# Performance work log

Hardware: AMD Instinct MI355X
Metric: run time of the kernel (lower is better)

## Reference

```python
import jax, jax.numpy as jnp
import numpy as np

B, S, D, H = 4, 2048, 1024, 16
HD = D // H  # head_dim = 64


def setup_inputs() -> dict:
    key = jax.random.key(0)
    ks = jax.random.split(key, 5)
    scale = 1.0 / np.sqrt(D)
    return {
        "x": jax.random.normal(ks[0], (B, S, D), dtype=jnp.float32),
        "Wq": jax.random.normal(ks[1], (D, D), dtype=jnp.float32) * scale,
        "bq": jnp.zeros((D,), dtype=jnp.float32),
        "Wk": jax.random.normal(ks[2], (D, D), dtype=jnp.float32) * scale,
        "bk": jnp.zeros((D,), dtype=jnp.float32),
        "Wv": jax.random.normal(ks[3], (D, D), dtype=jnp.float32) * scale,
        "bv": jnp.zeros((D,), dtype=jnp.float32),
        "Wp": jax.random.normal(ks[4], (D, D), dtype=jnp.float32) * scale,
        "bp": jnp.zeros((D,), dtype=jnp.float32),
    }


def reference(x, Wq, bq, Wk, bk, Wv, bv, Wp, bp):
    b, s, d = x.shape
    # qkv projections (torch Linear: x @ W.T + b; here W stored as (in,out))
    q = (x @ Wq + bq).reshape(b, s, H, HD).transpose(0, 2, 1, 3)  # (b,h,s,hd)
    k = (x @ Wk + bk).reshape(b, s, H, HD).transpose(0, 2, 1, 3)
    v = (x @ Wv + bv).reshape(b, s, H, HD).transpose(0, 2, 1, 3)
    scores = jnp.einsum("bhqd,bhkd->bhqk", q, k) / np.sqrt(HD)
    causal = jnp.tril(jnp.ones((s, s), dtype=bool))
    scores = jnp.where(causal, scores, -jnp.inf)
    attn = jax.nn.softmax(scores, axis=-1)  # dropout is identity (p=0 / eval)
    out = jnp.einsum("bhqk,bhkd->bhqd", attn, v)
    out = out.transpose(0, 2, 1, 3).reshape(b, s, d)
    return out @ Wp + bp
```

## Files before the change

### kernel.cpp

```cpp
#include <hip/hip_runtime.h>

typedef __bf16 bf16;
typedef __attribute__((ext_vector_type(4))) __bf16 bf16x4;
typedef __attribute__((ext_vector_type(8))) __bf16 bf16x8;
typedef __attribute__((ext_vector_type(4))) float f32x4;
typedef __attribute__((ext_vector_type(4))) unsigned int u32x4;

#define B_ 4
#define S_ 2048
#define D_ 1024
#define H_ 16
#define HD_ 64

#define GLB(p) ((const __attribute__((address_space(1))) void*)(p))
#define LDS(p) ((__attribute__((address_space(3))) void*)(p))

__global__ __launch_bounds__(256) void transpose_cvt(
    const float* __restrict__ W0, const float* __restrict__ W1,
    const float* __restrict__ W2, const float* __restrict__ W3,
    bf16* __restrict__ T0, bf16* __restrict__ T1,
    bf16* __restrict__ T2, bf16* __restrict__ T3)
{
    __shared__ float tile[32][33];
    int z = blockIdx.z;
    const float* W = (z == 0) ? W0 : (z == 1) ? W1 : (z == 2) ? W2 : W3;
    bf16*        T = (z == 0) ? T0 : (z == 1) ? T1 : (z == 2) ? T2 : T3;
    int bx = blockIdx.x * 32, by = blockIdx.y * 32;
    int tx = threadIdx.x & 31, ty = threadIdx.x >> 5;
    #pragma unroll
    for (int j = 0; j < 32; j += 8)
        tile[ty + j][tx] = W[(size_t)(by + ty + j) * D_ + bx + tx];
    __syncthreads();
    #pragma unroll
    for (int j = 0; j < 32; j += 8)
        T[(size_t)(bx + ty + j) * D_ + by + tx] = (bf16)tile[tx][ty + j];
}

__global__ __launch_bounds__(256) void cvt_x(
    const float* __restrict__ X, bf16* __restrict__ Xb)
{
    size_t i = ((size_t)blockIdx.x * 256 + threadIdx.x) * 8;
    f32x4 a = *(const f32x4*)(X + i);
    f32x4 b = *(const f32x4*)(X + i + 4);
    bf16x8 v;
    #pragma unroll
    for (int j = 0; j < 4; ++j) { v[j] = (bf16)a[j]; v[4 + j] = (bf16)b[j]; }
    *(bf16x8*)(Xb + i) = v;
}

__global__ __launch_bounds__(256) void qkv_gemm(
    const bf16* __restrict__ Xb,
    const bf16* __restrict__ WqT, const bf16* __restrict__ WkT, const bf16* __restrict__ WvT,
    const float* __restrict__ bq, const float* __restrict__ bk, const float* __restrict__ bv,
    bf16* __restrict__ Qo, bf16* __restrict__ Ko, bf16* __restrict__ Vo)
{
    const int lin = blockIdx.x + (blockIdx.y << 3) + (blockIdx.z << 9);
    const int xcd = lin & 7, rest = lin >> 3;
    const int byb = xcd * 8 + (rest & 7);
    const int bxb = (rest >> 3) & 7;
    const int z   = rest >> 6;

    const bf16*  WT   = (z == 0) ? WqT : (z == 1) ? WkT : WvT;
    const float* bias = (z == 0) ? bq  : (z == 1) ? bk  : bv;
    bf16*        out  = (z == 0) ? Qo  : (z == 1) ? Ko  : Vo;
    const float scale = (z == 0) ? 0.18033688011112042f : 1.0f;

    __shared__ bf16 As[128 * 64];
    __shared__ bf16 Bs[128 * 64];

    const int t = threadIdx.x;
    const int lid = t & 63, w = t >> 6;
    const int wm = w & 1, wn = w >> 1;
    const int lrow = lid & 15, quad = lid >> 4;
    const int m0 = byb * 128, n0 = bxb * 128;

    const bf16* Ag = Xb + (size_t)m0 * D_;
    const bf16* Bg = WT + (size_t)n0 * D_;

    const int srow = t >> 3;
    const int ssel = ((t & 7) ^ (srow & 7)) << 3;

    const int rsw = lrow & 7;

    f32x4 acc[4][4] = {};

    for (int k0 = 0; k0 < D_; k0 += 64) {
        __syncthreads();
        #pragma unroll
        for (int j = 0; j < 4; ++j) {
            __builtin_amdgcn_global_load_lds(
                GLB(Ag + (size_t)(srow + j * 32) * D_ + k0 + ssel),
                LDS((char*)As + j * 4096 + t * 16), 16, 0, 0);
            __builtin_amdgcn_global_load_lds(
                GLB(Bg + (size_t)(srow + j * 32) * D_ + k0 + ssel),
                LDS((char*)Bs + j * 4096 + t * 16), 16, 0, 0);
        }
        __syncthreads();
        #pragma unroll
        for (int kk = 0; kk < 2; ++kk) {
            const int ro = ((kk * 4 + quad) ^ rsw) << 4;
            bf16x8 a[4], b[4];
            #pragma unroll
            for (int mb = 0; mb < 4; ++mb)
                a[mb] = *(const bf16x8*)((const char*)As + (wm * 64 + mb * 16 + lrow) * 128 + ro);
            #pragma unroll
            for (int nb = 0; nb < 4; ++nb)
                b[nb] = *(const bf16x8*)((const char*)Bs + (wn * 64 + nb * 16 + lrow) * 128 + ro);
            #pragma unroll
            for (int mb = 0; mb < 4; ++mb)
                #pragma unroll
                for (int nb = 0; nb < 4; ++nb)
                    acc[mb][nb] = __builtin_amdgcn_mfma_f32_16x16x32_bf16(a[mb], b[nb], acc[mb][nb], 0, 0, 0);
        }
    }

    #pragma unroll
    for (int mb = 0; mb < 4; ++mb) {
        #pragma unroll
        for (int nb = 0; nb < 4; ++nb) {
            int gn = n0 + wn * 64 + nb * 16 + lrow;
            float bsv = bias[gn];
            int h = gn >> 6, hd = gn & 63;
            int gm0 = m0 + wm * 64 + mb * 16 + quad * 4;
            int bb = gm0 >> 11, s0 = gm0 & 2047;
            if (z == 2) {
                bf16x4 pk;
                #pragma unroll
                for (int r = 0; r < 4; ++r)
                    pk[r] = (bf16)(acc[mb][nb][r] + bsv);
                *(bf16x4*)(out + (((size_t)(bb * H_ + h)) * HD_ + hd) * S_ + s0) = pk;
            } else {
                #pragma unroll
                for (int r = 0; r < 4; ++r) {
                    float v = (acc[mb][nb][r] + bsv) * scale;
                    out[(((size_t)(bb * H_ + h)) * S_ + (s0 + r)) * HD_ + hd] = (bf16)v;
                }
            }
        }
    }
}

__global__ __launch_bounds__(256) void attn_fwd(
    const bf16* __restrict__ Q, const bf16* __restrict__ K,
    const bf16* __restrict__ Vt, bf16* __restrict__ O)
{
    __shared__ bf16 Ks[64 * 64];
    __shared__ bf16 Vs[64 * 64];
    __shared__ bf16 Ps[4][16 * 64];

    const int lin = blockIdx.x + (blockIdx.y << 4);
    const int xcd = lin & 7;
    const int sl  = lin >> 3;
    const int bh  = xcd * 8 + (sl >> 4);
    const int bxp = sl & 15;

    const int t = threadIdx.x, lid = t & 63, w = t >> 6;
    const int lrow = lid & 15, quad = lid >> 4;
    const int b = bh >> 4, h = bh & 15;

    const int swz = (lrow & 7) << 4;

    const int srow0 = t >> 3, srow1 = srow0 + 32;
    const int k8 = (t & 7) << 3;
    const int sswz = ((t & 7) << 4) ^ ((srow0 & 7) << 4);
    char* kdst0 = (char*)Ks + srow0 * 128 + sswz;
    char* kdst1 = (char*)Ks + srow1 * 128 + sswz;
    char* vdst0 = (char*)Vs + srow0 * 128 + sswz;
    char* vdst1 = (char*)Vs + srow1 * 128 + sswz;

    bf16x8 onesv;
    #pragma unroll
    for (int j = 0; j < 8; ++j) onesv[j] = (bf16)1.0f;

    #pragma unroll 1
    for (int half = 0; half < 2; ++half) {
        const int qtile = half ? bxp : (31 - bxp);
        const int qbase = qtile * 64;

        const bf16* Qp = Q + ((size_t)bh * S_ + qbase + w * 16) * HD_;
        bf16x8 qf[2];
        #pragma unroll
        for (int ks = 0; ks < 2; ++ks)
            qf[ks] = *(const bf16x8*)(Qp + lrow * HD_ + ks * 32 + quad * 8);

        f32x4 o_acc[4] = {};
        f32x4 l_acc = {0.0f, 0.0f, 0.0f, 0.0f};
        float m_i = -3.0e4f;

        for (int kt = 0; kt <= qtile; ++kt) {
            const bf16* Kp = K  + ((size_t)bh * S_ + kt * 64) * HD_;
            const bf16* Vp = Vt + ((size_t)bh * HD_) * S_ + kt * 64;
            __syncthreads();
            u32x4 kv0 = *(const u32x4*)(Kp + (size_t)srow0 * HD_ + k8);
            u32x4 kv1 = *(const u32x4*)(Kp + (size_t)srow1 * HD_ + k8);
            u32x4 vv0 = *(const u32x4*)(Vp + (size_t)srow0 * S_ + k8);
            u32x4 vv1 = *(const u32x4*)(Vp + (size_t)srow1 * S_ + k8);
            *(u32x4*)kdst0 = kv0;
            *(u32x4*)kdst1 = kv1;
            *(u32x4*)vdst0 = vv0;
            *(u32x4*)vdst1 = vv1;
            __syncthreads();

            f32x4 sa[4] = {};
            #pragma unroll
            for (int ks = 0; ks < 2; ++ks) {
                const int ro = ((ks << 6) + (quad << 4)) ^ swz;
                #pragma unroll
                for (int nb = 0; nb < 4; ++nb) {
                    bf16x8 kf = *(const bf16x8*)((const char*)Ks + (nb * 16 + lrow) * 128 + ro);
                    sa[nb] = __builtin_amdgcn_mfma_f32_16x16x32_bf16(kf, qf[ks], sa[nb], 0, 0, 0);
                }
            }

            if (kt == qtile) {
                int q = qbase + w * 16 + lrow;
                #pragma unroll
                for (int nb = 0; nb < 4; ++nb) {
                    int key = kt * 64 + nb * 16 + quad * 4;
                    #pragma unroll
                    for (int r = 0; r < 4; ++r)
                        if (key + r > q) sa[nb][r] = -3.0e4f;
                }
            }

            float p[4][4];
            {
                #pragma unroll
                for (int nb = 0; nb < 4; ++nb)
                    #pragma unroll
                    for (int r = 0; r < 4; ++r)
                        p[nb][r] = __builtin_amdgcn_exp2f(sa[nb][r] - m_i);

                float r0 = fmaxf(fmaxf(sa[0][0], sa[0][1]), sa[0][2]);
                float r1 = fmaxf(fmaxf(sa[0][3], sa[1][0]), sa[1][1]);
                float r2 = fmaxf(fmaxf(sa[1][2], sa[1][3]), sa[2][0]);
                float r3 = fmaxf(fmaxf(sa[2][1], sa[2][2]), sa[2][3]);
                float r4 = fmaxf(fmaxf(sa[3][0], sa[3][1]), sa[3][2]);
                float rm = fmaxf(fmaxf(fmaxf(r0, r1), r2),
                                 fmaxf(fmaxf(r3, r4), sa[3][3]));

                if (!__all(rm <= m_i + 8.0f)) {
                    rm = fmaxf(rm, __shfl_xor(rm, 16));
                    rm = fmaxf(rm, __shfl_xor(rm, 32));
                    float mnew = fmaxf(m_i, rm);
                    float al = __builtin_amdgcn_exp2f(m_i - mnew);
                    m_i = mnew;
                    #pragma unroll
                    for (int nb = 0; nb < 4; ++nb)
                        #pragma unroll
                        for (int r = 0; r < 4; ++r) {
                            o_acc[nb][r] *= al;
                            p[nb][r] = __builtin_amdgcn_exp2f(sa[nb][r] - m_i);
                        }
                    #pragma unroll
                    for (int r = 0; r < 4; ++r)
                        l_acc[r] *= al;
                }
            }

            char* pw = (char*)Ps[w] + lrow * 128;
            #pragma unroll
            for (int nb = 0; nb < 4; ++nb) {
                bf16x4 pk;
                #pragma unroll
                for (int r = 0; r < 4; ++r)
                    pk[r] = (bf16)p[nb][r];
                *(bf16x4*)(pw + ((nb * 32 + quad * 8) ^ swz)) = pk;
            }
            asm volatile("s_waitcnt lgkmcnt(0)" ::: "memory");

            #pragma unroll
            for (int ks = 0; ks < 2; ++ks) {
                const int ro = ((ks << 6) + (quad << 4)) ^ swz;
                bf16x8 pf = *(const bf16x8*)(pw + ro);
                #pragma unroll
                for (int nb = 0; nb < 4; ++nb) {
                    bf16x8 vf = *(const bf16x8*)((const char*)Vs + (nb * 16 + lrow) * 128 + ro);
                    o_acc[nb] = __builtin_amdgcn_mfma_f32_16x16x32_bf16(vf, pf, o_acc[nb], 0, 0, 0);
                }
                l_acc = __builtin_amdgcn_mfma_f32_16x16x32_bf16(onesv, pf, l_acc, 0, 0, 0);
            }
        }

        {
            float inv = 1.0f / l_acc[0];
            int s = qbase + w * 16 + lrow;
            #pragma unroll
            for (int nb = 0; nb < 4; ++nb) {
                bf16x4 pk;
                #pragma unroll
                for (int r = 0; r < 4; ++r)
                    pk[r] = (bf16)(o_acc[nb][r] * inv);
                *(bf16x4*)(O + ((size_t)b * S_ + s) * D_ + h * 64 + nb * 16 + quad * 4) = pk;
            }
        }
        __syncthreads();
    }
}

__global__ __launch_bounds__(256) void proj_gemm(
    const bf16* __restrict__ A, const bf16* __restrict__ WpT,
    const float* __restrict__ bp, float* __restrict__ out)
{
    const int lin = blockIdx.x + (blockIdx.y << 3);
    const int xcd = lin & 7, rest = lin >> 3;
    const int byb = xcd * 8 + (rest & 7);
    const int bxb = rest >> 3;

    __shared__ bf16 As[128 * 64];
    __shared__ bf16 Bs[128 * 64];

    const int t = threadIdx.x;
    const int lid = t & 63, w = t >> 6;
    const int wm = w & 1, wn = w >> 1;
    const int lrow = lid & 15, quad = lid >> 4;
    const int m0 = byb * 128, n0 = bxb * 128;

    const bf16* Ag = A   + (size_t)m0 * D_;
    const bf16* Bg = WpT + (size_t)n0 * D_;

    const int srow = t >> 3;
    const int ssel = ((t & 7) ^ (srow & 7)) << 3;
    const int rsw = lrow & 7;

    f32x4 acc[4][4] = {};

    for (int k0 = 0; k0 < D_; k0 += 64) {
        __syncthreads();
        #pragma unroll
        for (int j = 0; j < 4; ++j) {
            __builtin_amdgcn_global_load_lds(
                GLB(Ag + (size_t)(srow + j * 32) * D_ + k0 + ssel),
                LDS((char*)As + j * 4096 + t * 16), 16, 0, 0);
            __builtin_amdgcn_global_load_lds(
                GLB(Bg + (size_t)(srow + j * 32) * D_ + k0 + ssel),
                LDS((char*)Bs + j * 4096 + t * 16), 16, 0, 0);
        }
        __syncthreads();
        #pragma unroll
        for (int kk = 0; kk < 2; ++kk) {
            const int ro = ((kk * 4 + quad) ^ rsw) << 4;
            bf16x8 a[4], b[4];
            #pragma unroll
            for (int mb = 0; mb < 4; ++mb)
                a[mb] = *(const bf16x8*)((const char*)As + (wm * 64 + mb * 16 + lrow) * 128 + ro);
            #pragma unroll
            for (int nb = 0; nb < 4; ++nb)
                b[nb] = *(const bf16x8*)((const char*)Bs + (wn * 64 + nb * 16 + lrow) * 128 + ro);
            #pragma unroll
            for (int mb = 0; mb < 4; ++mb)
                #pragma unroll
                for (int nb = 0; nb < 4; ++nb)
                    acc[mb][nb] = __builtin_amdgcn_mfma_f32_16x16x32_bf16(a[mb], b[nb], acc[mb][nb], 0, 0, 0);
        }
    }

    #pragma unroll
    for (int mb = 0; mb < 4; ++mb) {
        #pragma unroll
        for (int nb = 0; nb < 4; ++nb) {
            int gn = n0 + wn * 64 + nb * 16 + lrow;
            float bsv = bp[gn];
            #pragma unroll
            for (int r = 0; r < 4; ++r) {
                int gm = m0 + wm * 64 + mb * 16 + quad * 4 + r;
                out[(size_t)gm * D_ + gn] = acc[mb][nb][r] + bsv;
            }
        }
    }
}

extern "C" void kernel_launch(void* const* d_in, const int* in_sizes, int n_in,
                              void* d_out, int out_size, void* d_ws, size_t ws_size,
                              hipStream_t stream)
{
    const float* x  = (const float*)d_in[0];
    const float* Wq = (const float*)d_in[1];
    const float* bq = (const float*)d_in[2];
    const float* Wk = (const float*)d_in[3];
    const float* bk = (const float*)d_in[4];
    const float* Wv = (const float*)d_in[5];
    const float* bv = (const float*)d_in[6];
    const float* Wp = (const float*)d_in[7];
    const float* bp = (const float*)d_in[8];

    bf16* ws = (bf16*)d_ws;
    const size_t WSZ = (size_t)D_ * D_;
    const size_t BIG = (size_t)B_ * S_ * D_;
    bf16* WqT = ws;
    bf16* WkT = WqT + WSZ;
    bf16* WvT = WkT + WSZ;
    bf16* WpT = WvT + WSZ;
    bf16* Qb  = WpT + WSZ;
    bf16* Kb  = Qb + BIG;
    bf16* Vb  = Kb + BIG;
    bf16* Ab  = Vb + BIG;

    transpose_cvt<<<dim3(32, 32, 4), 256, 0, stream>>>(
        Wq, Wk, Wv, Wp, WqT, WkT, WvT, WpT);

    cvt_x<<<dim3(4096), 256, 0, stream>>>(x, Ab);

    qkv_gemm<<<dim3(8, 64, 3), 256, 0, stream>>>(
        Ab, WqT, WkT, WvT, bq, bk, bv, Qb, Kb, Vb);

    attn_fwd<<<dim3(16, 64), 256, 0, stream>>>(Qb, Kb, Vb, Ab);

    proj_gemm<<<dim3(8, 64), 256, 0, stream>>>(Ab, WpT, bp, (float*)d_out);
}
```

Baseline: 256.7 us.

## Rewrite QKV GEMM with 256x256 tiles, 512 threads, double-buffered LDS pipeline

Replaces the 128x128 single-buffered QKV projection GEMM with a 256x256 tile kernel using 8 waves and double-buffered LDS. Global-to-LDS loads for the next K slices are issued in phases interleaved with MFMA work, using explicit vmcnt waits and barriers plus s_setprio around the MFMA blocks. It treats WqT/WkT/WvT as one contiguous 3072-wide weight matrix to remove per-z pointer selection. The aim is to hide load latency and raise data reuse, at the cost of more LDS (128KB per block), more registers and a fragile hand-written wait schedule.

```diff
diff --git a/kernel.cpp b/kernel.cpp
--- a/kernel.cpp
+++ b/kernel.cpp
@@ -48,80 +48,128 @@
     *(bf16x8*)(Xb + i) = v;
 }
 
-__global__ __launch_bounds__(256) void qkv_gemm(
-    const bf16* __restrict__ Xb,
-    const bf16* __restrict__ WqT, const bf16* __restrict__ WkT, const bf16* __restrict__ WvT,
+__global__ __launch_bounds__(512, 2) void qkv_gemm(
+    const bf16* __restrict__ Xb, const bf16* __restrict__ WqT,
     const float* __restrict__ bq, const float* __restrict__ bk, const float* __restrict__ bv,
     bf16* __restrict__ Qo, bf16* __restrict__ Ko, bf16* __restrict__ Vo)
 {
-    const int lin = blockIdx.x + (blockIdx.y << 3) + (blockIdx.z << 9);
-    const int xcd = lin & 7, rest = lin >> 3;
-    const int byb = xcd * 8 + (rest & 7);
-    const int bxb = (rest >> 3) & 7;
-    const int z   = rest >> 6;
-
-    const bf16*  WT   = (z == 0) ? WqT : (z == 1) ? WkT : WvT;
-    const float* bias = (z == 0) ? bq  : (z == 1) ? bk  : bv;
-    bf16*        out  = (z == 0) ? Qo  : (z == 1) ? Ko  : Vo;
+    __shared__ bf16 As[2][2][8192];
+    __shared__ bf16 Bs[2][2][8192];
+
+    const int lin = blockIdx.x;
+    const int xcd = lin & 7, rr = lin >> 3;
+    const int byb = xcd * 4 + (rr & 3);
+    const int bxb = rr >> 2;
+    const int m0 = byb * 256, n0 = bxb * 256;
+    const int z = bxb >> 2;
+
+    const float* bias = (z == 0) ? bq : (z == 1) ? bk : bv;
+    bf16*        out  = (z == 0) ? Qo : (z == 1) ? Ko : Vo;
     const float scale = (z == 0) ? 0.18033688011112042f : 1.0f;
-
-    __shared__ bf16 As[128 * 64];
-    __shared__ bf16 Bs[128 * 64];
 
     const int t = threadIdx.x;
     const int lid = t & 63, w = t >> 6;
     const int wm = w & 1, wn = w >> 1;
     const int lrow = lid & 15, quad = lid >> 4;
-    const int m0 = byb * 128, n0 = bxb * 128;
-
-    const bf16* Ag = Xb + (size_t)m0 * D_;
-    const bf16* Bg = WT + (size_t)n0 * D_;
-
-    const int srow = t >> 3;
-    const int ssel = ((t & 7) ^ (srow & 7)) << 3;
-
     const int rsw = lrow & 7;
 
-    f32x4 acc[4][4] = {};
-
-    for (int k0 = 0; k0 < D_; k0 += 64) {
-        __syncthreads();
-        #pragma unroll
-        for (int j = 0; j < 4; ++j) {
-            __builtin_amdgcn_global_load_lds(
-                GLB(Ag + (size_t)(srow + j * 32) * D_ + k0 + ssel),
-                LDS((char*)As + j * 4096 + t * 16), 16, 0, 0);
-            __builtin_amdgcn_global_load_lds(
-                GLB(Bg + (size_t)(srow + j * 32) * D_ + k0 + ssel),
-                LDS((char*)Bs + j * 4096 + t * 16), 16, 0, 0);
-        }
-        __syncthreads();
-        #pragma unroll
-        for (int kk = 0; kk < 2; ++kk) {
-            const int ro = ((kk * 4 + quad) ^ rsw) << 4;
-            bf16x8 a[4], b[4];
-            #pragma unroll
-            for (int mb = 0; mb < 4; ++mb)
-                a[mb] = *(const bf16x8*)((const char*)As + (wm * 64 + mb * 16 + lrow) * 128 + ro);
-            #pragma unroll
-            for (int nb = 0; nb < 4; ++nb)
-                b[nb] = *(const bf16x8*)((const char*)Bs + (wn * 64 + nb * 16 + lrow) * 128 + ro);
-            #pragma unroll
-            for (int mb = 0; mb < 4; ++mb)
-                #pragma unroll
-                for (int nb = 0; nb < 4; ++nb)
-                    acc[mb][nb] = __builtin_amdgcn_mfma_f32_16x16x32_bf16(a[mb], b[nb], acc[mb][nb], 0, 0, 0);
+    const int srow0 = t >> 3;
+    const int sc0 = ((t & 7) ^ (srow0 & 7)) << 3;
+
+    const bf16* aS[2] = { Xb  + (size_t)m0 * D_,        Xb  + (size_t)(m0 + 128) * D_ };
+    const bf16* bS[2] = { WqT + (size_t)n0 * D_,        WqT + (size_t)(n0 + 128) * D_ };
+
+    auto STG = [&](bf16* dst, const bf16* src) {
+        __builtin_amdgcn_global_load_lds(GLB(src + (size_t)srow0 * D_ + sc0),
+                                         LDS((char*)dst + (t << 4)), 16, 0, 0);
+        __builtin_amdgcn_global_load_lds(GLB(src + (size_t)(srow0 + 64) * D_ + sc0),
+                                         LDS((char*)dst + (t << 4) + 8192), 16, 0, 0);
+    };
+
+    f32x4 acc[8][4] = {};
+
+    STG(As[0][0], aS[0]); STG(As[0][1], aS[1]);
+    STG(Bs[0][0], bS[0]); STG(Bs[0][1], bS[1]);
+    asm volatile("s_waitcnt vmcnt(0)" ::: "memory");
+    asm volatile("s_barrier" ::: "memory");
+
+    #pragma unroll 1
+    for (int it = 0; it < 8; ++it) {
+        const bool lastit = (it == 7);
+        const int ko1 = (2 * it + 1) << 6;
+        const int ko2 = (2 * it + 2) << 6;
+
+        bf16x8 a[4][2];
+        bf16x8 bfr[4][2];
+
+        #pragma unroll
+        for (int ph = 0; ph < 8; ++ph) {
+            const int buf = ph >> 2;
+            const int sub = ph & 3;
+            const int qm = sub >> 1, qn = sub & 1;
+
+            if (ph == 0) STG(As[1][0], aS[0] + ko1);
+            if (ph == 1) STG(As[1][1], aS[1] + ko1);
+            if (ph == 2) STG(Bs[1][0], bS[0] + ko1);
+            if (ph == 3) STG(Bs[1][1], bS[1] + ko1);
+            if (!lastit) {
+                if (ph == 4) STG(As[0][0], aS[0] + ko2);
+                if (ph == 5) STG(As[0][1], aS[1] + ko2);
+                if (ph == 6) STG(Bs[0][0], bS[0] + ko2);
+                if (ph == 7) STG(Bs[0][1], bS[1] + ko2);
+            }
+
+            if (ph == 0) asm volatile("s_waitcnt vmcnt(2)" ::: "memory");
+            if (ph == 4) {
+                if (lastit) asm volatile("s_waitcnt vmcnt(0)" ::: "memory");
+                else        asm volatile("s_waitcnt vmcnt(2)" ::: "memory");
+            }
+            asm volatile("s_barrier" ::: "memory");
+
+            const char* Ah = (const char*)As[buf][wm];
+            const char* Bh = (const char*)Bs[buf][wn >> 1];
+            if (qn == 0) {
+                #pragma unroll
+                for (int m4 = 0; m4 < 4; ++m4)
+                    #pragma unroll
+                    for (int ks = 0; ks < 2; ++ks)
+                        a[m4][ks] = *(const bf16x8*)(Ah + (qm * 64 + m4 * 16 + lrow) * 128
+                                                        + ((((ks << 2) + quad) ^ rsw) << 4));
+            }
+            if (sub == 0 || sub == 1) {
+                #pragma unroll
+                for (int n2 = 0; n2 < 2; ++n2)
+                    #pragma unroll
+                    for (int ks = 0; ks < 2; ++ks)
+                        bfr[sub * 2 + n2][ks] = *(const bf16x8*)(Bh
+                            + ((wn & 1) * 64 + (sub * 2 + n2) * 16 + lrow) * 128
+                            + ((((ks << 2) + quad) ^ rsw) << 4));
+            }
+
+            __builtin_amdgcn_s_setprio(1);
+            #pragma unroll
+            for (int m4 = 0; m4 < 4; ++m4)
+                #pragma unroll
+                for (int n2 = 0; n2 < 2; ++n2) {
+                    f32x4 acv = acc[qm * 4 + m4][qn * 2 + n2];
+                    acv = __builtin_amdgcn_mfma_f32_16x16x32_bf16(a[m4][0], bfr[qn * 2 + n2][0], acv, 0, 0, 0);
+                    acv = __builtin_amdgcn_mfma_f32_16x16x32_bf16(a[m4][1], bfr[qn * 2 + n2][1], acv, 0, 0, 0);
+                    acc[qm * 4 + m4][qn * 2 + n2] = acv;
+                }
+            __builtin_amdgcn_s_setprio(0);
+            asm volatile("s_barrier" ::: "memory");
         }
     }
 
     #pragma unroll
-    for (int mb = 0; mb < 4; ++mb) {
+    for (int mb = 0; mb < 8; ++mb) {
         #pragma unroll
         for (int nb = 0; nb < 4; ++nb) {
             int gn = n0 + wn * 64 + nb * 16 + lrow;
-            float bsv = bias[gn];
-            int h = gn >> 6, hd = gn & 63;
-            int gm0 = m0 + wm * 64 + mb * 16 + quad * 4;
+            int nz = gn & 1023;
+            float bsv = bias[nz];
+            int h = nz >> 6, hd = nz & 63;
+            int gm0 = m0 + wm * 128 + mb * 16 + quad * 4;
             int bb = gm0 >> 11, s0 = gm0 & 2047;
             if (z == 2) {
                 bf16x4 pk;
@@ -401,8 +449,8 @@
 
     cvt_x<<<dim3(4096), 256, 0, stream>>>(x, Ab);
 
-    qkv_gemm<<<dim3(8, 64, 3), 256, 0, stream>>>(
-        Ab, WqT, WkT, WvT, bq, bk, bv, Qb, Kb, Vb);
+    qkv_gemm<<<dim3(384), 512, 0, stream>>>(
+        Ab, WqT, bq, bk, bv, Qb, Kb, Vb);
 
     attn_fwd<<<dim3(16, 64), 256, 0, stream>>>(Qb, Kb, Vb, Ab);
 
```

Result: slower. 264.3 us (+3.0%).
